# Kernel tuning notes

Hardware: AMD Instinct MI355X
Metric: run time of the kernel (lower is better)

The kernel has to match this reference:

```python
import jax, jax.numpy as jnp
import numpy as np

B, S, HD, NH, AH, F = 64, 256, 512, 8, 256, 2
DH = HD // NH          # item/pos head dim = 64
DA = AH // NH          # attribute head dim = 32
EPS = 1e-12


def setup_inputs() -> dict:
    key = jax.random.key(0)
    ks = iter(jax.random.split(key, 32))
    rn = lambda shape, s=1.0: jax.random.normal(next(ks), shape, dtype=jnp.float32) * s
    w = 0.02
    return {
        "input_tensor": rn((B, S, HD)),
        "attribute_table": rn((B, S, 1, AH)),
        "position_embedding": rn((B, S, HD)),
        "Wq": rn((HD, HD), w), "bq": jnp.zeros((HD,), jnp.float32),
        "Wk": rn((HD, HD), w), "bk": jnp.zeros((HD,), jnp.float32),
        "Wv": rn((HD, HD), w), "bv": jnp.zeros((HD,), jnp.float32),
        "Wqp": rn((HD, HD), w), "bqp": jnp.zeros((HD,), jnp.float32),
        "Wkp": rn((HD, HD), w), "bkp": jnp.zeros((HD,), jnp.float32),
        "Wqa": rn((F, AH, AH), w), "bqa": jnp.zeros((F, AH), jnp.float32),
        "Wka": rn((F, AH, AH), w), "bka": jnp.zeros((F, AH), jnp.float32),
        "fw1": rn((S, S), w), "fb1": jnp.zeros((S,), jnp.float32),
        "fw2": rn((1, S), w), "fb2": jnp.zeros((1,), jnp.float32),
        "Wd": rn((HD, HD), w), "bd": jnp.zeros((HD,), jnp.float32),
        "gamma": jnp.ones((HD,), jnp.float32),
        "beta": jnp.zeros((HD,), jnp.float32),
    }


def _split_heads(x, nh):
    b, s, h = x.shape
    return x.reshape(b, s, nh, h // nh).transpose(0, 2, 1, 3)  # [B,H,S,d]


def reference(input_tensor, attribute_table, position_embedding,
              Wq, bq, Wk, bk, Wv, bv, Wqp, bqp, Wkp, bkp,
              Wqa, bqa, Wka, bka, fw1, fb1, fw2, fb2,
              Wd, bd, gamma, beta):
    q = _split_heads(input_tensor @ Wq.T + bq, NH)
    k = _split_heads(input_tensor @ Wk.T + bk, NH)
    v = _split_heads(input_tensor @ Wv.T + bv, NH)
    qp = _split_heads(position_embedding @ Wqp.T + bqp, NH)
    kp = _split_heads(position_embedding @ Wkp.T + bkp, NH)

    item_scores = jnp.einsum('bhqd,bhkd->bhqk', q, k)
    pos_scores = jnp.einsum('bhqd,bhkd->bhqk', qp, kp)

    attr = attribute_table.squeeze(-2)                       # [B,S,AH]
    qa = jnp.einsum('bsc,foc->fbso', attr, Wqa) + bqa[:, None, None, :]
    ka = jnp.einsum('bsc,foc->fbso', attr, Wka) + bka[:, None, None, :]
    qa = qa.reshape(F, B, S, NH, DA).transpose(0, 1, 3, 2, 4)  # [F,B,H,S,da]
    ka = ka.reshape(F, B, S, NH, DA).transpose(0, 1, 3, 2, 4)
    attr_scores = jnp.einsum('fbhqd,fbhkd->fbhqk', qa, ka)
    attr_scores = attr_scores.transpose(1, 2, 3, 0, 4)         # [B,H,S,F,S]

    # gate fusion (VanillaAttention over the F+2 score sources)
    stacked = jnp.concatenate(
        [attr_scores, item_scores[..., None, :], pos_scores[..., None, :]],
        axis=-2)                                               # [B,H,S,F+2,S]
    energy = jnp.maximum(stacked @ fw1.T + fb1, 0.0) @ fw2.T + fb2
    gate_w = jax.nn.softmax(energy.squeeze(-1), axis=-1)        # [B,H,S,F+2]
    scores = jnp.sum(stacked * gate_w[..., None], axis=-2)      # [B,H,S,S]

    scores = scores / np.sqrt(DH).astype(np.float32)
    probs = jax.nn.softmax(scores, axis=-1)
    ctx = jnp.einsum('bhqk,bhkd->bhqd', probs, v)
    ctx = ctx.transpose(0, 2, 1, 3).reshape(B, S, HD)

    h = ctx @ Wd.T + bd
    x = h + input_tensor
    mu = jnp.mean(x, axis=-1, keepdims=True)
    var = jnp.mean(jnp.square(x - mu), axis=-1, keepdims=True)
    return gamma * (x - mu) / jnp.sqrt(var + EPS) + beta
```

## Files before the change

kernel.cpp:

```cpp
#include <hip/hip_runtime.h>

typedef unsigned short u16;
typedef unsigned int   u32;
typedef __bf16 bf16x8 __attribute__((ext_vector_type(8)));
typedef float  f32x4  __attribute__((ext_vector_type(4)));
typedef u16    u16x4  __attribute__((ext_vector_type(4)));
typedef u16    u16x8  __attribute__((ext_vector_type(8)));

#define BB 64
#define SS 256
#define HDIM 512
#define NHEAD 8
#define BS (BB*SS)
#define NBH 512

__device__ __forceinline__ u16 f2bf(float f){
    u32 u = __builtin_bit_cast(u32, f);
    u32 r = u + 0x7FFFu + ((u>>16)&1u);
    return (u16)(r>>16);
}
__device__ __forceinline__ float bf2f(u16 u){
    return __builtin_bit_cast(float, (u32)u<<16);
}
__device__ __forceinline__ void gload16(const void* g, void* l){
    __builtin_amdgcn_global_load_lds(
        (const __attribute__((address_space(1))) void*)g,
        (__attribute__((address_space(3))) void*)l, 16, 0, 0);
}

__device__ __forceinline__ size_t zrow(int bh, int s){
    return ((size_t)bh*256 + s)*384;
}

__global__ __launch_bounds__(256) void cvt_k(const float* __restrict__ s,
                                             u16* __restrict__ d, int n8)
{
    int i = blockIdx.x*256 + threadIdx.x;
    const int stride = gridDim.x*256;
    for (; i < n8; i += stride) {
        f32x4 a = ((const f32x4*)s)[i*2];
        f32x4 b = ((const f32x4*)s)[i*2+1];
        u16x8 o = { f2bf(a[0]),f2bf(a[1]),f2bf(a[2]),f2bf(a[3]),
                    f2bf(b[0]),f2bf(b[1]),f2bf(b[2]),f2bf(b[3]) };
        ((u16x8*)d)[i] = o;
    }
}

__global__ __launch_bounds__(256) void cvtW_k(
    const float* __restrict__ Wq,  const float* __restrict__ Wk,
    const float* __restrict__ Wv,  const float* __restrict__ Wqp,
    const float* __restrict__ Wkp, const float* __restrict__ Wqa,
    const float* __restrict__ Wka, const float* __restrict__ Wd,
    u16* __restrict__ dst)
{
    const int i = blockIdx.x*256 + threadIdx.x;
    const float* s; u16* d; int local;
    if (i < 163840) {
        const int seg = i >> 15; local = i & 32767;
        s = seg==0?Wq:seg==1?Wk:seg==2?Wv:seg==3?Wqp:Wkp;
        d = dst + (size_t)seg*262144;
    } else if (i < 196608) {
        const int j = i - 163840; const int seg = j >> 14; local = j & 16383;
        s = seg ? Wka : Wqa;
        d = dst + 1310720 + (size_t)seg*131072;
    } else {
        local = i - 196608;
        s = Wd; d = dst + 1572864;
    }
    f32x4 a = ((const f32x4*)s)[local*2];
    f32x4 b = ((const f32x4*)s)[local*2+1];
    u16x8 o = { f2bf(a[0]),f2bf(a[1]),f2bf(a[2]),f2bf(a[3]),
                f2bf(b[0]),f2bf(b[1]),f2bf(b[2]),f2bf(b[3]) };
    ((u16x8*)d)[local] = o;
}

__global__ __launch_bounds__(64) void prep_fw1(const float* __restrict__ fw1,
                                               u16* __restrict__ fw1f)
{
    const int j = blockIdx.x*2 + (threadIdx.x >> 5);
    const int t = threadIdx.x & 31;
    const int k0 = t*8;
    f32x4 a = *(const f32x4*)(fw1 + (size_t)j*256 + k0);
    f32x4 b = *(const f32x4*)(fw1 + (size_t)j*256 + k0 + 4);
    u16x8 o = { f2bf(a[0]),f2bf(a[1]),f2bf(a[2]),f2bf(a[3]),
                f2bf(b[0]),f2bf(b[1]),f2bf(b[2]),f2bf(b[3]) };
    const int jt = j >> 4, ks = t >> 2, lq = t & 3;
    ((u16x8*)fw1f)[(jt*8 + ks)*64 + lq*16 + (j & 15)] = o;
}

template<int OUTMODE, int BBF16>
__global__ __launch_bounds__(256,4) void gemm128(
    const u16* __restrict__ A, const void* __restrict__ Bv,
    void* __restrict__ o0, void* __restrict__ o1, void* __restrict__ o2,
    const float* __restrict__ b0, const float* __restrict__ b1,
    const float* __restrict__ b2, const float* __restrict__ resid,
    int N, int K)
{
    __shared__ char sA[16384];
    __shared__ char sB[16384];
    const int tid = threadIdx.x, lane = tid & 63, w = tid >> 6;
    const int wr = (w & 1) * 64, wc = (w >> 1) * 64;
    const int flat = blockIdx.x;
    const int xcd = flat & 7, bi2 = flat >> 3;
    const int n_i = bi2 >> 4, mIn = bi2 & 15;
    const int m0 = (xcd*16 + mIn)*128, n0 = n_i*128;

    f32x4 acc[4][4];
    #pragma unroll
    for (int mi = 0; mi < 4; mi++)
        #pragma unroll
        for (int ni = 0; ni < 4; ni++) acc[mi][ni] = (f32x4){0.f,0.f,0.f,0.f};

    for (int k0 = 0; k0 < K; k0 += 64) {
        __syncthreads();
        #pragma unroll
        for (int i = 0; i < 4; i++) {
            const int off = w*4096 + i*1024 + lane*16;
            const int r = off >> 7, c = off & 0x70;
            gload16(A + (size_t)(m0 + r)*K + k0 + ((c ^ ((r&7)<<4)) >> 1),
                    sA + w*4096 + i*1024);
        }
        if (BBF16) {
            const u16* B = (const u16*)Bv;
            #pragma unroll
            for (int i = 0; i < 4; i++) {
                const int off = w*4096 + i*1024 + lane*16;
                const int r = off >> 7, c = off & 0x70;
                gload16(B + (size_t)(n0 + r)*K + k0 + ((c ^ ((r&7)<<4)) >> 1),
                        sB + w*4096 + i*1024);
            }
        } else {
            const float* B = (const float*)Bv;
            const int r = tid >> 1, cseg = (tid & 1) * 32;
            const float* p = B + (size_t)(n0 + r)*K + k0 + cseg;
            alignas(16) u16 tmp[32];
            #pragma unroll
            for (int j = 0; j < 8; j++) {
                float4 fv = ((const float4*)p)[j];
                tmp[j*4+0]=f2bf(fv.x); tmp[j*4+1]=f2bf(fv.y);
                tmp[j*4+2]=f2bf(fv.z); tmp[j*4+3]=f2bf(fv.w);
            }
            const int rx = (r&7)<<4;
            #pragma unroll
            for (int j = 0; j < 4; j++)
                *(u16x8*)(sB + r*128 + ((cseg*2 + j*16) ^ rx)) = *(u16x8*)(tmp + j*8);
        }
        __syncthreads();
        #pragma unroll
        for (int ks = 0; ks < 2; ks++) {
            const int kb = ks*64 + (lane>>4)*16;
            bf16x8 af[4], bf[4];
            #pragma unroll
            for (int mi = 0; mi < 4; mi++) {
                const int r = wr + mi*16 + (lane&15);
                af[mi] = *(const bf16x8*)(sA + r*128 + (kb ^ ((r&7)<<4)));
            }
            #pragma unroll
            for (int ni = 0; ni < 4; ni++) {
                const int r = wc + ni*16 + (lane&15);
                bf[ni] = *(const bf16x8*)(sB + r*128 + (kb ^ ((r&7)<<4)));
            }
            #pragma unroll
            for (int mi = 0; mi < 4; mi++)
                #pragma unroll
                for (int ni = 0; ni < 4; ni++)
                    acc[mi][ni] = __builtin_amdgcn_mfma_f32_16x16x32_bf16(
                        af[mi], bf[ni], acc[mi][ni], 0,0,0);
        }
    }
    #pragma unroll
    for (int mi = 0; mi < 4; mi++) {
        const int rowb = m0 + wr + mi*16 + (lane>>4)*4;
        const int bi = rowb >> 8, s0 = rowb & 255;
        #pragma unroll
        for (int ni = 0; ni < 4; ni++) {
            const int gn = n0 + wc + ni*16 + (lane&15);
            if (OUTMODE == 2) {
                float* out = (float*)o0;
                const float bb = b0[gn];
                #pragma unroll
                for (int r = 0; r < 4; r++) {
                    size_t idx = (size_t)(rowb+r)*N + gn;
                    out[idx] = acc[mi][ni][r] + bb + resid[idx];
                }
            } else if (OUTMODE == 4) {
                const int seg = gn >> 9, o = gn & 511;
                const int hh = o >> 6, d = o & 63;
                const float bb = (seg==0?b0:seg==1?b1:b2)[o];
                const int bh = bi*8 + hh;
                if (seg < 2) {
                    char* outp = (char*)(seg ? o1 : o0);
                    #pragma unroll
                    for (int r = 0; r < 4; r++) {
                        const int s = s0 + r;
                        *(u16*)(outp + zrow(bh,s) + ((d*2) ^ ((s&7)<<4)))
                            = f2bf(acc[mi][ni][r] + bb);
                    }
                } else {
                    u16x4 pk;
                    #pragma unroll
                    for (int r = 0; r < 4; r++) pk[r] = f2bf(acc[mi][ni][r] + bb);
                    *(u16x4*)((char*)o2 + (size_t)bh*32768 + d*512
                                        + ((s0*2) ^ ((d&7)<<4))) = pk;
                }
            } else if (OUTMODE == 5) {
                const int seg = gn >> 9, o = gn & 511;
                const int hh = o >> 6, d = o & 63;
                const float bb = (seg ? b1 : b0)[o];
                const int bh = bi*8 + hh;
                char* outp = (char*)(seg ? o1 : o0);
                #pragma unroll
                for (int r = 0; r < 4; r++) {
                    const int s = s0 + r;
                    *(u16*)(outp + zrow(bh,s) + (((64+d)*2) ^ ((s&7)<<4)))
                        = f2bf(acc[mi][ni][r] + bb);
                }
            } else {
                const int qk = gn >> 9, fo = gn & 511;
                const int f = fo >> 8, o = fo & 255;
                const int hh = o >> 5, d = o & 31;
                const int cb = 128 + f*32;
                const float bb = (qk ? b1 : b0)[fo];
                const int bh = bi*8 + hh;
                char* outp = (char*)(qk ? o1 : o0);
                #pragma unroll
                for (int r = 0; r < 4; r++) {
                    const int s = s0 + r;
                    *(u16*)(outp + zrow(bh,s) + (((cb+d)*2) ^ ((s&7)<<4)))
                        = f2bf(acc[mi][ni][r] + bb);
                }
            }
        }
    }
}

#define K34B_QZ   53248
#define K34B_QZSZ 13312
#define K34B_SMEM (53248 + 2*13312)

__global__ __launch_bounds__(512,4) void k34b(
    const u16* __restrict__ QZ, const u16* __restrict__ KZ,
    const u16* __restrict__ fw1f, const float* __restrict__ fb1,
    const float* __restrict__ fw2, float* __restrict__ e)
{
    extern __shared__ char sm[];
    const int tid = threadIdx.x, lane = tid & 63, w = tid >> 6;
    const int bh = blockIdx.x >> 1, sp = blockIdx.x & 1;
    const int l15 = lane & 15, lq = lane >> 4;
    const int base0 = sp ? 64 : 0;
    const int base1 = sp ? 160 : 128;

    auto stage_qz = [&](int qt4, int buf) {
        char* dst = sm + K34B_QZ + buf*K34B_QZSZ;
        {
            const int li = w*64 + lane;
            const int q = li / 13, c = li - q*13;
            const int cc = (c == 12) ? 0 : c;
            const int ld = cc*8;
            const int gd = (ld < 64) ? base0 + ld : base1 + (ld - 64);
            gload16((const char*)QZ + zrow(bh, qt4*64 + q)
                        + ((gd*2) ^ ((q&7)<<4)),
                    dst + w*1024);
        }
        if (w < 5) {
            const int li = 512 + w*64 + lane;
            const int q = li / 13, c = li - q*13;
            const int cc = (c == 12) ? 0 : c;
            const int ld = cc*8;
            const int gd = (ld < 64) ? base0 + ld : base1 + (ld - 64);
            gload16((const char*)QZ + zrow(bh, qt4*64 + q)
                        + ((gd*2) ^ ((q&7)<<4)),
                    dst + 8192 + w*1024);
        }
    };

    stage_qz(0, 0);
    {
        const int spair = tid & 127, dg = tid >> 7;
        const int s0 = spair*2;
        const char* r0 = (const char*)KZ + zrow(bh, s0);
        const char* r1 = (const char*)KZ + zrow(bh, s0+1);
        const int sw0 = (s0&7)<<4, sw1 = ((s0+1)&7)<<4;
        #pragma unroll
        for (int m = 0; m < 3; m++) {
            const int ld0 = dg*24 + m*8;
            const int gd = (ld0 < 64) ? base0 + ld0 : base1 + (ld0 - 64);
            u16x8 v0 = *(const u16x8*)(r0 + ((gd*2) ^ sw0));
            u16x8 v1 = *(const u16x8*)(r1 + ((gd*2) ^ sw1));
            #pragma unroll
            for (int ee = 0; ee < 8; ee++) {
                const int d = ld0 + ee;
                *(u32*)(sm + d*512 + ((s0*2) ^ ((d&7)<<4)))
                    = (u32)v0[ee] | ((u32)v1[ee] << 16);
            }
        }
    }
    __syncthreads();

    const int jb = w & 3, dh = w >> 2;
    f32x4 kacc[4][3];
    #pragma unroll
    for (int js = 0; js < 4; js++)
        #pragma unroll
        for (int ni = 0; ni < 3; ni++) kacc[js][ni] = (f32x4){0.f,0.f,0.f,0.f};
    #pragma unroll
    for (int ks = 0; ks < 8; ks++) {
        const int kb = ks*64 + lq*16;
        bf16x8 a[4];
        #pragma unroll
        for (int js = 0; js < 4; js++)
            a[js] = ((const bf16x8*)fw1f)[((jb*4 + js)*8 + ks)*64 + lane];
        #pragma unroll
        for (int ni = 0; ni < 3; ni++) {
            const int dr = dh*48 + ni*16 + l15;
            bf16x8 b = *(const bf16x8*)(sm + dr*512 + (kb ^ ((dr&7)<<4)));
            #pragma unroll
            for (int js = 0; js < 4; js++)
                kacc[js][ni] = __builtin_amdgcn_mfma_f32_16x16x32_bf16(
                    a[js], b, kacc[js][ni], 0,0,0);
        }
    }
    __syncthreads();

    #pragma unroll
    for (int js = 0; js < 4; js++)
        #pragma unroll
        for (int ni = 0; ni < 3; ni++) {
            const int d = dh*48 + ni*16 + l15;
            #pragma unroll
            for (int r = 0; r < 4; r++) {
                const int j = jb*64 + js*16 + lq*4 + r;
                *(u16*)(sm + j*208 + d*2) = f2bf(kacc[js][ni][r]);
            }
        }
    __syncthreads();

    const int qh = w >> 2;
    bf16x8 af2[4][3];
    #pragma unroll
    for (int js = 0; js < 4; js++) {
        const int ar = jb*64 + js*16 + l15;
        #pragma unroll
        for (int ks = 0; ks < 3; ks++)
            af2[js][ks] = *(const bf16x8*)(sm + ar*208 + ks*64 + lq*16);
    }
    float f1v[4][4], f2v[4][4];
    #pragma unroll
    for (int js = 0; js < 4; js++)
        #pragma unroll
        for (int r = 0; r < 4; r++) {
            const int j = jb*64 + js*16 + lq*4 + r;
            f1v[js][r] = fb1[j]; f2v[js][r] = fw2[j];
        }

    for (int qt = 0; qt < 4; qt++) {
        __syncthreads();
        if (qt < 3) stage_qz(qt+1, (qt+1)&1);
        const char* qb = sm + K34B_QZ + (qt&1)*K34B_QZSZ;
        #pragma unroll
        for (int qs = 0; qs < 2; qs++) {
            const int qoff = (qh*32 + qs*16 + l15)*208 + lq*16;
            f32x4 acc[4];
            #pragma unroll
            for (int js = 0; js < 4; js++) acc[js] = (f32x4){0.f,0.f,0.f,0.f};
            #pragma unroll
            for (int kk = 0; kk < 2; kk++) {
                bf16x8 b = *(const bf16x8*)(qb + qoff + kk*64);
                #pragma unroll
                for (int js = 0; js < 4; js++)
                    acc[js] = __builtin_amdgcn_mfma_f32_16x16x32_bf16(
                        af2[js][kk], b, acc[js], 0,0,0);
            }
            {
                float ep = 0.f;
                #pragma unroll
                for (int js = 0; js < 4; js++)
                    #pragma unroll
                    for (int r = 0; r < 4; r++)
                        ep += fmaxf(acc[js][r] + f1v[js][r], 0.f) * f2v[js][r];
                ep += __shfl_xor(ep, 16);
                ep += __shfl_xor(ep, 32);
                if (lane < 16)
                    ((float*)sm)[(jb*2 + 0)*256 + qt*64 + qh*32 + qs*16 + lane] = ep;
            }
            #pragma unroll
            for (int js = 0; js < 4; js++) acc[js] = (f32x4){0.f,0.f,0.f,0.f};
            {
                bf16x8 b = *(const bf16x8*)(qb + qoff + 128);
                #pragma unroll
                for (int js = 0; js < 4; js++)
                    acc[js] = __builtin_amdgcn_mfma_f32_16x16x32_bf16(
                        af2[js][2], b, acc[js], 0,0,0);
            }
            {
                float ep = 0.f;
                #pragma unroll
                for (int js = 0; js < 4; js++)
                    #pragma unroll
                    for (int r = 0; r < 4; r++)
                        ep += fmaxf(acc[js][r] + f1v[js][r], 0.f) * f2v[js][r];
                ep += __shfl_xor(ep, 16);
                ep += __shfl_xor(ep, 32);
                if (lane < 16)
                    ((float*)sm)[(jb*2 + 1)*256 + qt*64 + qh*32 + qs*16 + lane] = ep;
            }
        }
    }
    __syncthreads();
    {
        const int q = tid & 255, sl = tid >> 8;
        const float* el = (const float*)sm;
        float s = 0.f;
        #pragma unroll
        for (int j2 = 0; j2 < 4; j2++) s += el[(j2*2 + sl)*256 + q];
        const int gsrc = sl ? (2 + sp) : sp;
        e[((size_t)bh*256 + q)*4 + gsrc] = s;
    }
}

#define K5_KZ 24576
#define K5_VT 36864
#define K5_SMEM 53248

__global__ __launch_bounds__(256,3) void k5b(
    const u16* __restrict__ QZ, const u16* __restrict__ KZ,
    const u16* __restrict__ VT, const float* __restrict__ e,
    u16* __restrict__ ctx)
{
    extern __shared__ char sm[];
    const int tid = threadIdx.x, lane = tid & 63, w = tid >> 6;
    const int flat = blockIdx.x;
    const int xcd = flat & 7, idx = flat >> 3;
    const int qt = idx & 3;
    const int bh = (idx >> 2) * 8 + xcd;
    const int q0 = qt*64;
    const int b = bh >> 3, h = bh & 7;
    const int kq16 = (lane>>4)*16;
    const char* QZc = (const char*)QZ + zrow(bh, q0);
    const char* KZc = (const char*)KZ + zrow(bh, 0);
    const char* VTc = (const char*)VT + (size_t)bh*32768;

    #pragma unroll
    for (int i = 0; i < 6; i++)
        gload16(QZc + i*4096 + tid*16, sm + i*4096 + tid*16);
    #pragma unroll
    for (int i = 0; i < 3; i++)
        gload16(KZc + i*4096 + tid*16, sm + K5_KZ + i*4096 + tid*16);
    #pragma unroll
    for (int i = 0; i < 2; i++)
        gload16(VTc + i*4096 + tid*16, sm + K5_VT + i*4096 + tid*16);
    __syncthreads();

    const int qrow = w*16 + (lane&15);
    float ga[4];
    {
        f32x4 ev = *(const f32x4*)(e + ((size_t)bh*256 + q0 + qrow)*4);
        float em = fmaxf(fmaxf(ev[0],ev[1]), fmaxf(ev[2],ev[3]));
        float s = 0.f;
        #pragma unroll
        for (int j = 0; j < 4; j++) { ga[j] = __expf(ev[j]-em); s += ga[j]; }
        const float gi = 1.f / s;
        #pragma unroll
        for (int j = 0; j < 4; j++) ga[j] *= gi;
    }
    const int asw = ((lane&15)&7) << 4;
    bf16x8 aF[6];
    #pragma unroll
    for (int ks = 0; ks < 6; ks++) {
        const int sidx = (ks<2)?0:(ks<4)?1:(ks<5)?2:3;
        u16x8 v = *(const u16x8*)(sm + qrow*384 + ((ks*64 + kq16) ^ asw));
        const float gg = ga[sidx];
        u16x8 pk;
        #pragma unroll
        for (int j = 0; j < 8; j++) pk[j] = f2bf(bf2f(v[j]) * gg);
        aF[ks] = __builtin_bit_cast(bf16x8, pk);
    }

    f32x4 macc[16];
    #pragma unroll
    for (int t = 0; t < 16; t++) macc[t] = (f32x4){0.f,0.f,0.f,0.f};
    u16x8 kreg[3];
    #pragma unroll
    for (int kt = 0; kt < 8; kt++) {
        if (kt < 7) {
            #pragma unroll
            for (int j = 0; j < 3; j++)
                kreg[j] = *(const u16x8*)(KZc + (size_t)(kt+1)*12288
                                          + (tid + j*256)*16);
        }
        #pragma unroll
        for (int n2 = 0; n2 < 2; n2++) {
            const int kr = n2*16 + (lane&15);
            const int ksw = (kr&7)<<4;
            #pragma unroll
            for (int ks = 0; ks < 6; ks++) {
                bf16x8 bb = *(const bf16x8*)(sm + K5_KZ + kr*384
                                             + ((ks*64 + kq16) ^ ksw));
                macc[kt*2+n2] = __builtin_amdgcn_mfma_f32_16x16x32_bf16(
                    aF[ks], bb, macc[kt*2+n2], 0,0,0);
            }
        }
        if (kt < 7) {
            __syncthreads();
            #pragma unroll
            for (int j = 0; j < 3; j++)
                *(u16x8*)(sm + K5_KZ + (tid + j*256)*16) = kreg[j];
            __syncthreads();
        }
    }
    __syncthreads();

    #pragma unroll
    for (int rr = 0; rr < 4; rr++) {
        float mx = -3.4e38f;
        #pragma unroll
        for (int t = 0; t < 16; t++) mx = fmaxf(mx, macc[t][rr]);
        #pragma unroll
        for (int msk = 1; msk < 16; msk <<= 1) mx = fmaxf(mx, __shfl_xor(mx, msk));
        float s = 0.f;
        #pragma unroll
        for (int t = 0; t < 16; t++) {
            float pv = __expf((macc[t][rr] - mx) * 0.125f);
            macc[t][rr] = pv; s += pv;
        }
        #pragma unroll
        for (int msk = 1; msk < 16; msk <<= 1) s += __shfl_xor(s, msk);
        const float inv = 1.f / s;
        const int orow = w*16 + (lane>>4)*4 + rr;
        const int osw = (orow&7)<<4;
        #pragma unroll
        for (int t = 0; t < 16; t++) {
            const int col = t*16 + (lane&15);
            *(u16*)(sm + orow*512 + ((col*2) ^ osw)) = f2bf(macc[t][rr]*inv);
        }
    }
    __syncthreads();

    bf16x8 a[8];
    const int prow = w*16 + (lane&15);
    const int psw = ((lane&15)&7)<<4;
    #pragma unroll
    for (int ks = 0; ks < 8; ks++)
        a[ks] = *(const bf16x8*)(sm + prow*512 + ((ks*64 + kq16) ^ psw));

    const int orow = w*16 + (lane>>4)*4;
    #pragma unroll
    for (int n = 0; n < 4; n++) {
        if (n < 3) {
            #pragma unroll
            for (int i = 0; i < 2; i++)
                gload16(VTc + (size_t)(n+1)*8192 + i*4096 + tid*16,
                        sm + K5_VT + ((n+1)&1)*8192 + i*4096 + tid*16);
        }
        f32x4 pacc = (f32x4){0.f,0.f,0.f,0.f};
        const char* vb = sm + K5_VT + (n&1)*8192;
        const int dl = lane & 15;
        const int vsw = (dl&7)<<4;
        #pragma unroll
        for (int ks = 0; ks < 8; ks++) {
            bf16x8 bb = *(const bf16x8*)(vb + dl*512 + ((ks*64 + kq16) ^ vsw));
            pacc = __builtin_amdgcn_mfma_f32_16x16x32_bf16(a[ks], bb, pacc, 0,0,0);
        }
        {
            const int d = n*16 + dl;
            #pragma unroll
            for (int r = 0; r < 4; r++) {
                const size_t grow = (size_t)b*256 + q0 + orow + r;
                ctx[grow*512 + h*64 + d] = f2bf(pacc[r]);
            }
        }
        if (n < 3) __syncthreads();
    }
}

__global__ __launch_bounds__(256) void ln_k(float* __restrict__ x,
    const float* __restrict__ gamma, const float* __restrict__ beta)
{
    const int row = blockIdx.x*4 + (threadIdx.x >> 6);
    const int l = threadIdx.x & 63;
    float* p = x + (size_t)row*HDIM;
    f32x4 v0 = *(const f32x4*)(p + l*4);
    f32x4 v1 = *(const f32x4*)(p + 256 + l*4);
    float s = v0[0]+v0[1]+v0[2]+v0[3] + v1[0]+v1[1]+v1[2]+v1[3];
    #pragma unroll
    for (int msk = 1; msk < 64; msk <<= 1) s += __shfl_xor(s, msk);
    const float mu = s * (1.f/512.f);
    float vs = 0.f;
    #pragma unroll
    for (int j = 0; j < 4; j++) {
        float d0 = v0[j]-mu, d1 = v1[j]-mu;
        vs += d0*d0 + d1*d1;
    }
    #pragma unroll
    for (int msk = 1; msk < 64; msk <<= 1) vs += __shfl_xor(vs, msk);
    const float inv = 1.f / sqrtf(vs * (1.f/512.f) + 1e-12f);
    f32x4 o0, o1;
    #pragma unroll
    for (int j = 0; j < 4; j++) {
        o0[j] = gamma[l*4+j]     * (v0[j]-mu) * inv + beta[l*4+j];
        o1[j] = gamma[256+l*4+j] * (v1[j]-mu) * inv + beta[256+l*4+j];
    }
    *(f32x4*)(p + l*4) = o0;
    *(f32x4*)(p + 256 + l*4) = o1;
}

extern "C" void kernel_launch(void* const* d_in, const int* in_sizes, int n_in,
                              void* d_out, int out_size, void* d_ws, size_t ws_size,
                              hipStream_t stream)
{
    const float* input = (const float*)d_in[0];
    const float* attrt = (const float*)d_in[1];
    const float* pose  = (const float*)d_in[2];
    const float* Wq  = (const float*)d_in[3];  const float* bq  = (const float*)d_in[4];
    const float* Wk  = (const float*)d_in[5];  const float* bk  = (const float*)d_in[6];
    const float* Wv  = (const float*)d_in[7];  const float* bv  = (const float*)d_in[8];
    const float* Wqp = (const float*)d_in[9];  const float* bqp = (const float*)d_in[10];
    const float* Wkp = (const float*)d_in[11]; const float* bkp = (const float*)d_in[12];
    const float* Wqa = (const float*)d_in[13]; const float* bqa = (const float*)d_in[14];
    const float* Wka = (const float*)d_in[15]; const float* bka = (const float*)d_in[16];
    const float* fw1 = (const float*)d_in[17]; const float* fb1 = (const float*)d_in[18];
    const float* fw2 = (const float*)d_in[19];
    const float* Wd  = (const float*)d_in[21]; const float* bd  = (const float*)d_in[22];
    const float* gamma = (const float*)d_in[23]; const float* beta = (const float*)d_in[24];

    char* ws = (char*)d_ws;
    u16*   wsQZ  = (u16*)(ws);
    u16*   wsKZ  = (u16*)(ws + 50331648);
    u16*   wsTmp = (u16*)(ws + 100663296);
    float* wsE   = (float*)(ws + 117440512);
    u16*   fw1b  = (u16*)(ws + 119537664);
    u16*   dW    = (u16*)(ws + 119668736);
    u16*   wsVT  = (u16*)d_out;

    dim3 blk(256);

    cvtW_k<<<dim3(896), blk, 0, stream>>>(Wq, Wk, Wv, Wqp, Wkp, Wqa, Wka, Wd, dW);
    prep_fw1<<<dim3(128), dim3(64), 0, stream>>>(fw1, fw1b);

    cvt_k<<<dim3(2048), blk, 0, stream>>>(attrt, wsTmp, 524288);
    gemm128<6,1><<<dim3(1024), blk, 0, stream>>>(wsTmp, dW + 1310720,
        wsQZ, wsKZ, nullptr, bqa, bka, nullptr, nullptr, 1024, 256);
    cvt_k<<<dim3(2048), blk, 0, stream>>>(input, wsTmp, 1048576);
    gemm128<4,1><<<dim3(1536), blk, 0, stream>>>(wsTmp, dW,
        wsQZ, wsKZ, wsVT, bq, bk, bv, nullptr, 1536, 512);
    cvt_k<<<dim3(2048), blk, 0, stream>>>(pose, wsTmp, 1048576);
    gemm128<5,1><<<dim3(1024), blk, 0, stream>>>(wsTmp, dW + 786432,
        wsQZ, wsKZ, nullptr, bqp, bkp, nullptr, nullptr, 1024, 512);

    hipFuncSetAttribute(reinterpret_cast<const void*>(k34b),
                        hipFuncAttributeMaxDynamicSharedMemorySize, K34B_SMEM);
    k34b<<<dim3(NBH*2), dim3(512), K34B_SMEM, stream>>>(wsQZ, wsKZ, fw1b, fb1, fw2, wsE);

    hipFuncSetAttribute(reinterpret_cast<const void*>(k5b),
                        hipFuncAttributeMaxDynamicSharedMemorySize, K5_SMEM);
    k5b<<<dim3(2048), blk, K5_SMEM, stream>>>(wsQZ, wsKZ, wsVT, wsE, wsTmp);

    gemm128<2,1><<<dim3(512), blk, 0, stream>>>(wsTmp, dW + 1572864,
        d_out, nullptr, nullptr, bd, nullptr, nullptr, input, 512, 512);
    ln_k<<<dim3(BS/4), blk, 0, stream>>>((float*)d_out, gamma, beta);
}
```

Baseline: 233.2 us.

## Double-buffer GEMM shared-memory tiles and defer softmax normalization to output

```diff
diff --git a/kernel.cpp b/kernel.cpp
--- a/kernel.cpp
+++ b/kernel.cpp
@@ -89,15 +89,15 @@
 }
 
 template<int OUTMODE, int BBF16>
-__global__ __launch_bounds__(256,4) void gemm128(
+__global__ __launch_bounds__(256,2) void gemm128(
     const u16* __restrict__ A, const void* __restrict__ Bv,
     void* __restrict__ o0, void* __restrict__ o1, void* __restrict__ o2,
     const float* __restrict__ b0, const float* __restrict__ b1,
     const float* __restrict__ b2, const float* __restrict__ resid,
     int N, int K)
 {
-    __shared__ char sA[16384];
-    __shared__ char sB[16384];
+    __shared__ char sA[2][16384];
+    __shared__ char sB[2][16384];
     const int tid = threadIdx.x, lane = tid & 63, w = tid >> 6;
     const int wr = (w & 1) * 64, wc = (w >> 1) * 64;
     const int flat = blockIdx.x;
@@ -111,14 +111,13 @@
         #pragma unroll
         for (int ni = 0; ni < 4; ni++) acc[mi][ni] = (f32x4){0.f,0.f,0.f,0.f};
 
-    for (int k0 = 0; k0 < K; k0 += 64) {
-        __syncthreads();
+    auto stage = [&](int k0, int buf) {
         #pragma unroll
         for (int i = 0; i < 4; i++) {
             const int off = w*4096 + i*1024 + lane*16;
             const int r = off >> 7, c = off & 0x70;
             gload16(A + (size_t)(m0 + r)*K + k0 + ((c ^ ((r&7)<<4)) >> 1),
-                    sA + w*4096 + i*1024);
+                    sA[buf] + w*4096 + i*1024);
         }
         if (BBF16) {
             const u16* B = (const u16*)Bv;
@@ -127,7 +126,7 @@
                 const int off = w*4096 + i*1024 + lane*16;
                 const int r = off >> 7, c = off & 0x70;
                 gload16(B + (size_t)(n0 + r)*K + k0 + ((c ^ ((r&7)<<4)) >> 1),
-                        sB + w*4096 + i*1024);
+                        sB[buf] + w*4096 + i*1024);
             }
         } else {
             const float* B = (const float*)Bv;
@@ -143,9 +142,17 @@
             const int rx = (r&7)<<4;
             #pragma unroll
             for (int j = 0; j < 4; j++)
-                *(u16x8*)(sB + r*128 + ((cseg*2 + j*16) ^ rx)) = *(u16x8*)(tmp + j*8);
-        }
-        __syncthreads();
+                *(u16x8*)(sB[buf] + r*128 + ((cseg*2 + j*16) ^ rx))
+                    = *(u16x8*)(tmp + j*8);
+        }
+    };
+
+    stage(0, 0);
+    __syncthreads();
+    const int nk = K >> 6;
+    for (int kt = 0; kt < nk; kt++) {
+        const int cur = kt & 1;
+        if (kt + 1 < nk) stage((kt+1)*64, cur ^ 1);
         #pragma unroll
         for (int ks = 0; ks < 2; ks++) {
             const int kb = ks*64 + (lane>>4)*16;
@@ -153,12 +160,12 @@
             #pragma unroll
             for (int mi = 0; mi < 4; mi++) {
                 const int r = wr + mi*16 + (lane&15);
-                af[mi] = *(const bf16x8*)(sA + r*128 + (kb ^ ((r&7)<<4)));
+                af[mi] = *(const bf16x8*)(sA[cur] + r*128 + (kb ^ ((r&7)<<4)));
             }
             #pragma unroll
             for (int ni = 0; ni < 4; ni++) {
                 const int r = wc + ni*16 + (lane&15);
-                bf[ni] = *(const bf16x8*)(sB + r*128 + (kb ^ ((r&7)<<4)));
+                bf[ni] = *(const bf16x8*)(sB[cur] + r*128 + (kb ^ ((r&7)<<4)));
             }
             #pragma unroll
             for (int mi = 0; mi < 4; mi++)
@@ -167,6 +174,7 @@
                     acc[mi][ni] = __builtin_amdgcn_mfma_f32_16x16x32_bf16(
                         af[mi], bf[ni], acc[mi][ni], 0,0,0);
         }
+        __syncthreads();
     }
     #pragma unroll
     for (int mi = 0; mi < 4; mi++) {
@@ -510,6 +518,7 @@
     }
     __syncthreads();
 
+    float invs[4];
     #pragma unroll
     for (int rr = 0; rr < 4; rr++) {
         float mx = -3.4e38f;
@@ -525,13 +534,13 @@
         }
         #pragma unroll
         for (int msk = 1; msk < 16; msk <<= 1) s += __shfl_xor(s, msk);
-        const float inv = 1.f / s;
+        invs[rr] = 1.f / s;
         const int orow = w*16 + (lane>>4)*4 + rr;
         const int osw = (orow&7)<<4;
         #pragma unroll
         for (int t = 0; t < 16; t++) {
             const int col = t*16 + (lane&15);
-            *(u16*)(sm + orow*512 + ((col*2) ^ osw)) = f2bf(macc[t][rr]*inv);
+            *(u16*)(sm + orow*512 + ((col*2) ^ osw)) = f2bf(macc[t][rr]);
         }
     }
     __syncthreads();
@@ -566,7 +575,7 @@
             #pragma unroll
             for (int r = 0; r < 4; r++) {
                 const size_t grow = (size_t)b*256 + q0 + orow + r;
-                ctx[grow*512 + h*64 + d] = f2bf(pacc[r]);
+                ctx[grow*512 + h*64 + d] = f2bf(pacc[r] * invs[r]);
             }
         }
         if (n < 3) __syncthreads();
```

New measurement: 237.9 us. 2.1% more time.

## Fuse output dense projection with residual add and LayerNorm in one kernel

Applied to the files above, without the earlier changes.

```diff
diff --git a/kernel.cpp b/kernel.cpp
--- a/kernel.cpp
+++ b/kernel.cpp
@@ -175,15 +175,7 @@
         #pragma unroll
         for (int ni = 0; ni < 4; ni++) {
             const int gn = n0 + wc + ni*16 + (lane&15);
-            if (OUTMODE == 2) {
-                float* out = (float*)o0;
-                const float bb = b0[gn];
-                #pragma unroll
-                for (int r = 0; r < 4; r++) {
-                    size_t idx = (size_t)(rowb+r)*N + gn;
-                    out[idx] = acc[mi][ni][r] + bb + resid[idx];
-                }
-            } else if (OUTMODE == 4) {
+            if (OUTMODE == 4) {
                 const int seg = gn >> 9, o = gn & 511;
                 const int hh = o >> 6, d = o & 63;
                 const float bb = (seg==0?b0:seg==1?b1:b2)[o];
@@ -234,6 +226,108 @@
     }
 }
 
+#define GLN_SB   4096
+#define GLN_ST   69632
+#define GLN_SMEM 70144
+
+__global__ __launch_bounds__(256,2) void gemm_ln(
+    const u16* __restrict__ A, const u16* __restrict__ B,
+    const float* __restrict__ bd, const float* __restrict__ resid,
+    const float* __restrict__ gamma, const float* __restrict__ beta,
+    float* __restrict__ out)
+{
+    extern __shared__ char sm[];
+    char* sA = sm;
+    char* sB = sm + GLN_SB;
+    float* stats = (float*)(sm + GLN_ST);
+    const int tid = threadIdx.x, lane = tid & 63, w = tid >> 6;
+    const int l15 = lane & 15, lq = lane >> 4;
+    const int flat = blockIdx.x;
+    const int xcd = flat & 7, bi2 = flat >> 3;
+    const int m0 = (xcd*64 + bi2)*32;
+    const int wr = (w & 1)*16, wc2 = (w >> 1);
+
+    f32x4 acc[16];
+    #pragma unroll
+    for (int ni = 0; ni < 16; ni++) acc[ni] = (f32x4){0.f,0.f,0.f,0.f};
+
+    for (int k0 = 0; k0 < 512; k0 += 64) {
+        __syncthreads();
+        {
+            const int off = tid*16;
+            const int r = off >> 7, c = off & 0x70;
+            gload16(A + (size_t)(m0 + r)*512 + k0 + ((c ^ ((r&7)<<4)) >> 1),
+                    sA + tid*16);
+        }
+        #pragma unroll
+        for (int i = 0; i < 16; i++) {
+            const int off = i*4096 + tid*16;
+            const int r = off >> 7, c = off & 0x70;
+            gload16(B + (size_t)r*512 + k0 + ((c ^ ((r&7)<<4)) >> 1),
+                    sB + i*4096 + tid*16);
+        }
+        __syncthreads();
+        #pragma unroll
+        for (int ks = 0; ks < 2; ks++) {
+            const int kb = ks*64 + lq*16;
+            const int ra = wr + l15;
+            bf16x8 af = *(const bf16x8*)(sA + ra*128 + (kb ^ ((ra&7)<<4)));
+            #pragma unroll
+            for (int ni = 0; ni < 16; ni++) {
+                const int rb = wc2*256 + ni*16 + l15;
+                bf16x8 bf = *(const bf16x8*)(sB + rb*128 + (kb ^ ((rb&7)<<4)));
+                acc[ni] = __builtin_amdgcn_mfma_f32_16x16x32_bf16(
+                    af, bf, acc[ni], 0,0,0);
+            }
+        }
+    }
+
+    const int rowb = m0 + wr + lq*4;
+    float psum[4] = {0.f,0.f,0.f,0.f}, psq[4] = {0.f,0.f,0.f,0.f};
+    #pragma unroll
+    for (int ni = 0; ni < 16; ni++) {
+        const int col = wc2*256 + ni*16 + l15;
+        const float bb = bd[col];
+        #pragma unroll
+        for (int r = 0; r < 4; r++) {
+            float x = acc[ni][r] + bb + resid[(size_t)(rowb+r)*512 + col];
+            acc[ni][r] = x;
+            psum[r] += x; psq[r] += x*x;
+        }
+    }
+    #pragma unroll
+    for (int r = 0; r < 4; r++)
+        #pragma unroll
+        for (int msk = 1; msk < 16; msk <<= 1) {
+            psum[r] += __shfl_xor(psum[r], msk);
+            psq[r]  += __shfl_xor(psq[r],  msk);
+        }
+    if (l15 == 0) {
+        #pragma unroll
+        for (int r = 0; r < 4; r++) {
+            const int lrow = wr + lq*4 + r;
+            stats[(wc2*32 + lrow)*2 + 0] = psum[r];
+            stats[(wc2*32 + lrow)*2 + 1] = psq[r];
+        }
+    }
+    __syncthreads();
+    #pragma unroll
+    for (int r = 0; r < 4; r++) {
+        const int lrow = wr + lq*4 + r;
+        const float s  = stats[lrow*2]     + stats[(32+lrow)*2];
+        const float sq = stats[lrow*2 + 1] + stats[(32+lrow)*2 + 1];
+        const float mu  = s * (1.f/512.f);
+        const float var = sq * (1.f/512.f) - mu*mu;
+        const float inv = 1.f / sqrtf(var + 1e-12f);
+        #pragma unroll
+        for (int ni = 0; ni < 16; ni++) {
+            const int col = wc2*256 + ni*16 + l15;
+            out[(size_t)(rowb+r)*512 + col] =
+                gamma[col]*(acc[ni][r]-mu)*inv + beta[col];
+        }
+    }
+}
+
 #define K34B_QZ   53248
 #define K34B_QZSZ 13312
 #define K34B_SMEM (53248 + 2*13312)
@@ -571,37 +665,6 @@
         }
         if (n < 3) __syncthreads();
     }
-}
-
-__global__ __launch_bounds__(256) void ln_k(float* __restrict__ x,
-    const float* __restrict__ gamma, const float* __restrict__ beta)
-{
-    const int row = blockIdx.x*4 + (threadIdx.x >> 6);
-    const int l = threadIdx.x & 63;
-    float* p = x + (size_t)row*HDIM;
-    f32x4 v0 = *(const f32x4*)(p + l*4);
-    f32x4 v1 = *(const f32x4*)(p + 256 + l*4);
-    float s = v0[0]+v0[1]+v0[2]+v0[3] + v1[0]+v1[1]+v1[2]+v1[3];
-    #pragma unroll
-    for (int msk = 1; msk < 64; msk <<= 1) s += __shfl_xor(s, msk);
-    const float mu = s * (1.f/512.f);
-    float vs = 0.f;
-    #pragma unroll
-    for (int j = 0; j < 4; j++) {
-        float d0 = v0[j]-mu, d1 = v1[j]-mu;
-        vs += d0*d0 + d1*d1;
-    }
-    #pragma unroll
-    for (int msk = 1; msk < 64; msk <<= 1) vs += __shfl_xor(vs, msk);
-    const float inv = 1.f / sqrtf(vs * (1.f/512.f) + 1e-12f);
-    f32x4 o0, o1;
-    #pragma unroll
-    for (int j = 0; j < 4; j++) {
-        o0[j] = gamma[l*4+j]     * (v0[j]-mu) * inv + beta[l*4+j];
-        o1[j] = gamma[256+l*4+j] * (v1[j]-mu) * inv + beta[256+l*4+j];
-    }
-    *(f32x4*)(p + l*4) = o0;
-    *(f32x4*)(p + 256 + l*4) = o1;
 }
 
 extern "C" void kernel_launch(void* const* d_in, const int* in_sizes, int n_in,
@@ -655,7 +718,8 @@
                         hipFuncAttributeMaxDynamicSharedMemorySize, K5_SMEM);
     k5b<<<dim3(2048), blk, K5_SMEM, stream>>>(wsQZ, wsKZ, wsVT, wsE, wsTmp);
 
-    gemm128<2,1><<<dim3(512), blk, 0, stream>>>(wsTmp, dW + 1572864,
-        d_out, nullptr, nullptr, bd, nullptr, nullptr, input, 512, 512);
-    ln_k<<<dim3(BS/4), blk, 0, stream>>>((float*)d_out, gamma, beta);
-}
+    hipFuncSetAttribute(reinterpret_cast<const void*>(gemm_ln),
+                        hipFuncAttributeMaxDynamicSharedMemorySize, GLN_SMEM);
+    gemm_ln<<<dim3(512), blk, GLN_SMEM, stream>>>(wsTmp, dW + 1572864,
+        bd, input, gamma, beta, (float*)d_out);
+}
```

New measurement: 235.0 us. About the same (+0.8%).
